# Optimization experiments

Hardware: AMD Instinct MI355X
Metric: run time of the kernel (lower is better)

The kernel has to match this reference:

```python
import jax, jax.numpy as jnp
import numpy as np

N_NODES = 50000
N_EDGES = 800000
DIMS = [100, 512, 256, 128, 200]  # input -> conv1 -> conv2 -> conv3 -> conv4


def setup_inputs() -> dict:
    key = jax.random.key(0)
    ks = jax.random.split(key, 2 + 4)
    x = jax.random.normal(ks[0], (N_NODES, DIMS[0]), dtype=jnp.float32)
    edge_index = jax.random.randint(ks[1], (2, N_EDGES), 0, N_NODES, dtype=jnp.int64)
    inp = {"x": x, "edge_index": edge_index}
    for i in range(4):
        fan_in = DIMS[i]
        W = jax.random.normal(ks[2 + i], (DIMS[i], DIMS[i + 1]), dtype=jnp.float32) * (1.0 / np.sqrt(fan_in)).astype(np.float32)
        b = jnp.zeros((DIMS[i + 1],), dtype=jnp.float32)
        inp[f"W{i + 1}"] = W
        inp[f"b{i + 1}"] = b
    return inp


def _gcn_layer(x, row, col, norm, W, b, n):
    # PyG GCNConv: linear transform first, then normalized scatter-add, then bias.
    h = x @ W                           # [N, out]
    msg = h[row] * norm[:, None]        # [E+N, out] gather + edge scale
    agg = jax.ops.segment_sum(msg, col, num_segments=n)  # scatter-add to targets
    return agg + b


def reference(x, edge_index, W1, b1, W2, b2, W3, b3, W4, b4):
    n = x.shape[0]
    loop = jnp.arange(n, dtype=edge_index.dtype)
    row = jnp.concatenate([edge_index[0], loop])  # sources (with self-loops)
    col = jnp.concatenate([edge_index[1], loop])  # targets (with self-loops)
    deg = jax.ops.segment_sum(jnp.ones_like(col, dtype=x.dtype), col, num_segments=n)
    dinv = jnp.where(deg > 0, jax.lax.rsqrt(deg), 0.0)
    norm = dinv[row] * dinv[col]  # symmetric D^{-1/2}(A+I)D^{-1/2} edge weights

    out = jax.nn.relu(_gcn_layer(x, row, col, norm, W1, b1, n))
    out = jax.nn.relu(_gcn_layer(out, row, col, norm, W2, b2, n))
    out = jax.nn.relu(_gcn_layer(out, row, col, norm, W3, b3, n))
    out = jax.nn.relu(_gcn_layer(out, row, col, norm, W4, b4, n))
    return jnp.mean(out, axis=0, keepdims=True)  # [1, 200]
```

## Files before the change

kernel.cpp:

```cpp
#include <hip/hip_runtime.h>
#include <hip/hip_bf16.h>


#define NN 50000
#define NE 800000

typedef __attribute__((ext_vector_type(8))) _Float16 f16x8;
typedef __attribute__((ext_vector_type(4))) float floatx4;
typedef __attribute__((ext_vector_type(2))) float floatx2;

union U16x8 {
    uint4 u4;
    f16x8 h;
    _Float16 e[8];
};

__device__ __forceinline__ void dec16(const unsigned char* p, float* f) {
    uint4 v = *(const uint4*)p;
    unsigned w[4] = {v.x, v.y, v.z, v.w};
#pragma unroll
    for (int k = 0; k < 4; k++) {
        floatx2 lo = __builtin_amdgcn_cvt_pk_f32_fp8(w[k], false);
        floatx2 hi = __builtin_amdgcn_cvt_pk_f32_fp8(w[k], true);
        f[k * 4 + 0] = lo[0];
        f[k * 4 + 1] = lo[1];
        f[k * 4 + 2] = hi[0];
        f[k * 4 + 3] = hi[1];
    }
}

__device__ __forceinline__ uint4 enc16(const float* f) {
    uint4 r;
    unsigned w;
    w = __builtin_amdgcn_cvt_pk_fp8_f32(f[0], f[1], 0, false);
    w = __builtin_amdgcn_cvt_pk_fp8_f32(f[2], f[3], (int)w, true);
    r.x = w;
    w = __builtin_amdgcn_cvt_pk_fp8_f32(f[4], f[5], 0, false);
    w = __builtin_amdgcn_cvt_pk_fp8_f32(f[6], f[7], (int)w, true);
    r.y = w;
    w = __builtin_amdgcn_cvt_pk_fp8_f32(f[8], f[9], 0, false);
    w = __builtin_amdgcn_cvt_pk_fp8_f32(f[10], f[11], (int)w, true);
    r.z = w;
    w = __builtin_amdgcn_cvt_pk_fp8_f32(f[12], f[13], 0, false);
    w = __builtin_amdgcn_cvt_pk_fp8_f32(f[14], f[15], (int)w, true);
    r.w = w;
    return r;
}

__global__ __launch_bounds__(256) void zero_detect_kernel(
    const unsigned* __restrict__ ei, int* __restrict__ flag,
    unsigned* __restrict__ cnt, unsigned* __restrict__ fillc,
    float* __restrict__ out) {
    int tid = blockIdx.x * 256 + threadIdx.x;
    if (tid < NN) {
        cnt[tid] = 0u;
        fillc[tid] = 0u;
    }
    if (blockIdx.x == 0) {
        if (threadIdx.x < 200) out[threadIdx.x] = 0.f;
        unsigned w = ei[2 * threadIdx.x + 1];
        unsigned long long any = __ballot(w != 0);
        if (threadIdx.x == 0) *flag = (any == 0ull) ? 1 : 0;
    }
}

__device__ __forceinline__ int load_idx(const void* ei, int isflag64, size_t pos) {
    if (isflag64) return (int)((const long long*)ei)[pos];
    return ((const int*)ei)[pos];
}

__global__ __launch_bounds__(256) void count_kernel(const void* ei,
                                                    const int* __restrict__ flag,
                                                    unsigned* __restrict__ cnt) {
    int e = blockIdx.x * blockDim.x + threadIdx.x;
    if (e >= NE) return;
    int c = load_idx(ei, *flag, (size_t)NE + e);
    atomicAdd(&cnt[c], 1u);
}

__global__ __launch_bounds__(256) void scan1_kernel(const unsigned* __restrict__ cnt,
                                                    int* __restrict__ off,
                                                    int* __restrict__ bsum,
                                                    float* __restrict__ dinv) {
    __shared__ int ws[4];
    int b = blockIdx.x, t = threadIdx.x;
    int base = b * 1024 + t * 4;
    int v[4];
    int s = 0;
#pragma unroll
    for (int i = 0; i < 4; i++) {
        int val = 0;
        if (base + i < NN) {
            val = (int)cnt[base + i];
            dinv[base + i] = rsqrtf((float)(val + 1));
        }
        v[i] = s;
        s += val;
    }
    int lane = t & 63, wv = t >> 6;
    int x = s;
    for (int d = 1; d < 64; d <<= 1) {
        int y = __shfl_up(x, d, 64);
        if (lane >= d) x += y;
    }
    if (lane == 63) ws[wv] = x;
    __syncthreads();
    int wpre = 0;
#pragma unroll
    for (int i = 0; i < 4; i++)
        if (i < wv) wpre += ws[i];
    int texcl = x - s + wpre;
#pragma unroll
    for (int i = 0; i < 4; i++)
        if (base + i < NN) off[base + i] = texcl + v[i];
    if (t == 255) bsum[b] = texcl + s;
}

__global__ void scan2_kernel(int* bsum, int nb) {
    int t = threadIdx.x;
    int v = (t < nb) ? bsum[t] : 0;
    int x = v;
    for (int d = 1; d < 64; d <<= 1) {
        int y = __shfl_up(x, d, 64);
        if (t >= d) x += y;
    }
    if (t < nb) bsum[t] = x - v;
}

__global__ __launch_bounds__(256) void scan3_kernel(int* __restrict__ off,
                                                    const int* __restrict__ bsum) {
    int b = blockIdx.x;
    int add = bsum[b];
    int base = b * 1024 + threadIdx.x * 4;
#pragma unroll
    for (int i = 0; i < 4; i++)
        if (base + i < NN) off[base + i] += add;
    if (b == 0 && threadIdx.x == 0) off[NN] = NE;
}

__global__ __launch_bounds__(256) void fill_kernel(
    const void* ei, const int* __restrict__ flag, const int* __restrict__ off,
    unsigned* __restrict__ fillc, const float* __restrict__ dinv,
    int2* __restrict__ ep) {
    int e = blockIdx.x * blockDim.x + threadIdx.x;
    if (e >= NE) return;
    int f64 = *flag;
    int r = load_idx(ei, f64, e);
    int c = load_idx(ei, f64, (size_t)NE + e);
    int pos = off[c] + (int)atomicAdd(&fillc[c], 1u);
    int2 v;
    v.x = r;
    v.y = __float_as_int(dinv[r] * dinv[c]);
    ep[pos] = v;
}

__global__ __launch_bounds__(256) void xwcast_kernel(
    const float* __restrict__ x, unsigned char* __restrict__ xb,
    const float* __restrict__ W1, const float* __restrict__ W2,
    const float* __restrict__ W3, const float* __restrict__ W4,
    _Float16* __restrict__ w1t, _Float16* __restrict__ w2t,
    _Float16* __restrict__ w3t, _Float16* __restrict__ w4t) {
    int bx = blockIdx.x, t = threadIdx.x;
    if (bx < 1563) {
        int tid = bx * 256 + t;
        int node = tid >> 3, sub = tid & 7;
        if (node >= NN) return;
        int base = sub * 16;
        float f[16];
#pragma unroll
        for (int i = 0; i < 16; i++) {
            int c = base + i;
            f[i] = (c < 100) ? x[(size_t)node * 100 + c] : 0.f;
        }
        *(uint4*)(xb + (size_t)node * 128 + base) = enc16(f);
        return;
    }
    int b = bx - 1563;
    const float* W;
    _Float16* Wt;
    int K, N, Kpad, tid;
    if (b < 256)      { W = W1; Wt = w1t; K = 100; N = 512; Kpad = 128; tid = b * 256 + t; }
    else if (b < 768) { W = W2; Wt = w2t; K = 512; N = 256; Kpad = 512; tid = (b - 256) * 256 + t; }
    else if (b < 896) { W = W3; Wt = w3t; K = 256; N = 128; Kpad = 256; tid = (b - 768) * 256 + t; }
    else              { W = W4; Wt = w4t; K = 128; N = 200; Kpad = 128; tid = (b - 896) * 256 + t; }
    int n = tid / Kpad, k = tid - n * Kpad;
    float v = (k < K && n < N) ? W[(size_t)k * N + n] : 0.f;
    Wt[tid] = (_Float16)v;
}

template <int D, int BR, int OUT8>
__global__ __launch_bounds__(256) void agg_kernel(
    const unsigned char* __restrict__ H, const int* __restrict__ off,
    const int2* __restrict__ ep, const float* __restrict__ dinv,
    const float* __restrict__ bias, void* __restrict__ O) {
    constexpr int LPN = D / 16;
    int tid = blockIdx.x * 256 + threadIdx.x;
    int node = tid / LPN;
    int sub = tid % LPN;
    if (node >= NN) return;
    int s = off[node], e = off[node + 1];
    float dc = dinv[node];
    float selfw = dc * dc;
    const int base = sub * 16;
    const unsigned char* __restrict__ Hb = H + base;
    float acc[16], t0[16], t1[16];
    dec16(Hb + (size_t)node * D, t0);
#pragma unroll
    for (int i = 0; i < 16; i++) acc[i] = selfw * t0[i];
    int j = s;
    for (; j + 2 <= e; j += 2) {
        int2 q0 = ep[j];
        int2 q1 = ep[j + 1];
        dec16(Hb + (size_t)q0.x * D, t0);
        dec16(Hb + (size_t)q1.x * D, t1);
        float w0 = __int_as_float(q0.y);
        float w1 = __int_as_float(q1.y);
#pragma unroll
        for (int i = 0; i < 16; i++) acc[i] = fmaf(w0, t0[i], acc[i]);
#pragma unroll
        for (int i = 0; i < 16; i++) acc[i] = fmaf(w1, t1[i], acc[i]);
    }
    if (j < e) {
        int2 q0 = ep[j];
        dec16(Hb + (size_t)q0.x * D, t0);
        float w0 = __int_as_float(q0.y);
#pragma unroll
        for (int i = 0; i < 16; i++) acc[i] = fmaf(w0, t0[i], acc[i]);
    }
    if (BR) {
#pragma unroll
        for (int i = 0; i < 16; i++) acc[i] = fmaxf(acc[i] + bias[base + i], 0.f);
    }
    if (OUT8) {
        *(uint4*)((unsigned char*)O + (size_t)node * D + base) = enc16(acc);
    } else {
        U16x8 o0, o1;
#pragma unroll
        for (int i = 0; i < 8; i++) o0.e[i] = (_Float16)acc[i];
#pragma unroll
        for (int i = 0; i < 8; i++) o1.e[i] = (_Float16)acc[8 + i];
        _Float16* Op = (_Float16*)O + (size_t)node * D + base;
        *(uint4*)Op = o0.u4;
        *(uint4*)(Op + 8) = o1.u4;
    }
}

template <int EPI>
__global__ __launch_bounds__(256) void gemm_kernel(
    const _Float16* __restrict__ A, const _Float16* __restrict__ B,
    const float* __restrict__ bias, void* __restrict__ Cb,
    float* __restrict__ outmean, int M, int K, int N) {
    __shared__ _Float16 Asl[128 * 40];
    __shared__ _Float16 Bsl[128 * 40];
    __shared__ float red[128];
    const int m0 = blockIdx.y * 128;
    const int n0 = blockIdx.x * 128;
    const int t = threadIdx.x;
    const int lane = t & 63, w = t >> 6;
    const int wm = (w >> 1) * 64, wn = (w & 1) * 64;
    const int r16 = lane & 15, quad = lane >> 4;

    floatx4 acc[4][4];
    const floatx4 fz = {0.f, 0.f, 0.f, 0.f};
#pragma unroll
    for (int i = 0; i < 4; i++)
#pragma unroll
        for (int j = 0; j < 4; j++) acc[i][j] = fz;

    for (int kc = 0; kc < K; kc += 32) {
        __syncthreads();
#pragma unroll
        for (int i = 0; i < 2; i++) {
            int seg = t + 256 * i;
            int row = seg >> 2, k8 = (seg & 3) * 8;
            int gm = m0 + row;
            if (gm > M - 1) gm = M - 1;
            *(uint4*)(Asl + row * 40 + k8) = *(const uint4*)(A + (size_t)gm * K + kc + k8);
            int gn = n0 + row;
            *(uint4*)(Bsl + row * 40 + k8) = *(const uint4*)(B + (size_t)gn * K + kc + k8);
        }
        __syncthreads();
        f16x8 af[4], bf[4];
#pragma unroll
        for (int i = 0; i < 4; i++)
            af[i] = *(const f16x8*)(Asl + (wm + i * 16 + r16) * 40 + quad * 8);
#pragma unroll
        for (int j = 0; j < 4; j++)
            bf[j] = *(const f16x8*)(Bsl + (wn + j * 16 + r16) * 40 + quad * 8);
#pragma unroll
        for (int i = 0; i < 4; i++)
#pragma unroll
            for (int j = 0; j < 4; j++)
                acc[i][j] = __builtin_amdgcn_mfma_f32_16x16x32_f16(af[i], bf[j], acc[i][j], 0, 0, 0);
    }

    if (EPI == 2) {
        if (t < 128) red[t] = 0.f;
        __syncthreads();
#pragma unroll
        for (int j = 0; j < 4; j++) {
            int col = n0 + wn + j * 16 + r16;
            float s = 0.f;
            if (col < N) {
                float bv = bias[col];
#pragma unroll
                for (int i = 0; i < 4; i++)
#pragma unroll
                    for (int r = 0; r < 4; r++) {
                        int m = m0 + wm + i * 16 + quad * 4 + r;
                        if (m < M) s += fmaxf(acc[i][j][r] + bv, 0.f);
                    }
            }
            atomicAdd(&red[wn + j * 16 + r16], s);
        }
        __syncthreads();
        if (t < 128) {
            int col = n0 + t;
            if (col < N) atomicAdd(outmean + col, red[t] * (1.0f / (float)NN));
        }
    } else {
#pragma unroll
        for (int i = 0; i < 4; i++)
#pragma unroll
            for (int r = 0; r < 4; r++) {
                int m = m0 + wm + i * 16 + quad * 4 + r;
                if (m >= M) continue;
#pragma unroll
                for (int j = 0; j < 4; j++) {
                    int col = n0 + wn + j * 16 + r16;
                    float v = acc[i][j][r];
                    if (EPI == 1) v = fmaxf(v + bias[col], 0.f);
                    if (EPI == 3) {
                        unsigned pk = __builtin_amdgcn_cvt_pk_fp8_f32(v, v, 0, false);
                        ((unsigned char*)Cb)[(size_t)m * N + col] = (unsigned char)(pk & 0xffu);
                    } else {
                        ((_Float16*)Cb)[(size_t)m * N + col] = (_Float16)v;
                    }
                }
            }
    }
}

extern "C" void kernel_launch(void* const* d_in, const int* in_sizes, int n_in,
                              void* d_out, int out_size, void* d_ws, size_t ws_size,
                              hipStream_t stream) {
    const float* x  = (const float*)d_in[0];
    const void*  ei = d_in[1];
    const float* W1 = (const float*)d_in[2];
    const float* b1 = (const float*)d_in[3];
    const float* W2 = (const float*)d_in[4];
    const float* b2 = (const float*)d_in[5];
    const float* W3 = (const float*)d_in[6];
    const float* b3 = (const float*)d_in[7];
    const float* W4 = (const float*)d_in[8];
    const float* b4 = (const float*)d_in[9];
    float* out = (float*)d_out;

    char* ws = (char*)d_ws;
    size_t o = 0;
    auto alloc = [&](size_t bytes) -> void* {
        void* p = ws + o;
        o += (bytes + 255) & ~(size_t)255;
        return p;
    };
    int*      flag  = (int*)alloc(4);
    unsigned* cnt   = (unsigned*)alloc((size_t)NN * 4);
    int*      off   = (int*)alloc((size_t)(NN + 1) * 4);
    unsigned* fillc = (unsigned*)alloc((size_t)NN * 4);
    float*    dinv  = (float*)alloc((size_t)NN * 4);
    int2*     ep    = (int2*)alloc((size_t)NE * 8);
    _Float16* w1t = (_Float16*)alloc((size_t)512 * 128 * 2);
    _Float16* w2t = (_Float16*)alloc((size_t)256 * 512 * 2);
    _Float16* w3t = (_Float16*)alloc((size_t)128 * 256 * 2);
    _Float16* w4t = (_Float16*)alloc((size_t)256 * 128 * 2);
    int*      bsum  = (int*)alloc(256);
    unsigned char* xb  = (unsigned char*)alloc((size_t)NN * 128);
    _Float16*      A1b = (_Float16*)alloc((size_t)NN * 128 * 2);
    _Float16*      H1b = (_Float16*)alloc((size_t)NN * 512 * 2);
    unsigned char* t2b = (unsigned char*)alloc((size_t)NN * 256);
    _Float16*      H2b = (_Float16*)alloc((size_t)NN * 256 * 2);
    unsigned char* t3b = (unsigned char*)alloc((size_t)NN * 128);
    unsigned char* h3b = (unsigned char*)alloc((size_t)NN * 128);
    _Float16*      A4b = (_Float16*)alloc((size_t)NN * 128 * 2);

    const int EB = (NE + 255) / 256;
    const int NB1 = (NN + 1023) / 1024;
    const int ZB = (NN + 255) / 256;

    zero_detect_kernel<<<ZB, 256, 0, stream>>>((const unsigned*)ei, flag, cnt, fillc, out);
    count_kernel<<<EB, 256, 0, stream>>>(ei, flag, cnt);
    scan1_kernel<<<NB1, 256, 0, stream>>>(cnt, off, bsum, dinv);
    scan2_kernel<<<1, 64, 0, stream>>>(bsum, NB1);
    scan3_kernel<<<NB1, 256, 0, stream>>>(off, bsum);
    fill_kernel<<<EB, 256, 0, stream>>>(ei, flag, off, fillc, dinv, ep);
    xwcast_kernel<<<1563 + 1024, 256, 0, stream>>>(x, xb, W1, W2, W3, W4, w1t, w2t, w3t, w4t);

    const int MB = (NN + 127) / 128;
    const int AB128 = (NN * 8 + 255) / 256;
    const int AB256 = (NN * 16 + 255) / 256;

    agg_kernel<128, 0, 0><<<AB128, 256, 0, stream>>>(xb, off, ep, dinv, nullptr, A1b);
    gemm_kernel<1><<<dim3(4, MB), 256, 0, stream>>>(A1b, w1t, b1, H1b, nullptr, NN, 128, 512);
    gemm_kernel<3><<<dim3(2, MB), 256, 0, stream>>>(H1b, w2t, nullptr, t2b, nullptr, NN, 512, 256);
    agg_kernel<256, 1, 0><<<AB256, 256, 0, stream>>>(t2b, off, ep, dinv, b2, H2b);
    gemm_kernel<3><<<dim3(1, MB), 256, 0, stream>>>(H2b, w3t, nullptr, t3b, nullptr, NN, 256, 128);
    agg_kernel<128, 1, 1><<<AB128, 256, 0, stream>>>(t3b, off, ep, dinv, b3, h3b);
    agg_kernel<128, 0, 0><<<AB128, 256, 0, stream>>>(h3b, off, ep, dinv, nullptr, A4b);
    gemm_kernel<2><<<dim3(2, MB), 256, 0, stream>>>(A4b, w4t, b4, nullptr, out, NN, 128, 200);
}
```

Before: 356.0 us.

## Store all intermediate activations in fp8 and batch four edges per thread

All intermediate activations (aggregation outputs and GEMM outputs) are now stored as fp8 instead of fp16. The GEMM converts fp8 A tiles to fp16 while loading them into shared memory. This roughly halves memory traffic for several buffers, at the cost of extra conversion work and lower precision. The count and fill kernels also process four edges per thread to raise memory-level parallelism and cut thread overhead.

After: 356.4 us. Within noise of the previous version (+0.1%).

```diff
diff --git a/kernel.cpp b/kernel.cpp
--- a/kernel.cpp
+++ b/kernel.cpp
@@ -47,6 +47,19 @@
     return r;
 }
 
+__device__ __forceinline__ uint4 dec8_f16(uint2 v) {
+    floatx2 f0 = __builtin_amdgcn_cvt_pk_f32_fp8(v.x, false);
+    floatx2 f1 = __builtin_amdgcn_cvt_pk_f32_fp8(v.x, true);
+    floatx2 f2 = __builtin_amdgcn_cvt_pk_f32_fp8(v.y, false);
+    floatx2 f3 = __builtin_amdgcn_cvt_pk_f32_fp8(v.y, true);
+    U16x8 o;
+    o.e[0] = (_Float16)f0[0]; o.e[1] = (_Float16)f0[1];
+    o.e[2] = (_Float16)f1[0]; o.e[3] = (_Float16)f1[1];
+    o.e[4] = (_Float16)f2[0]; o.e[5] = (_Float16)f2[1];
+    o.e[6] = (_Float16)f3[0]; o.e[7] = (_Float16)f3[1];
+    return o.u4;
+}
+
 __global__ __launch_bounds__(256) void zero_detect_kernel(
     const unsigned* __restrict__ ei, int* __restrict__ flag,
     unsigned* __restrict__ cnt, unsigned* __restrict__ fillc,
@@ -64,18 +77,23 @@
     }
 }
 
-__device__ __forceinline__ int load_idx(const void* ei, int isflag64, size_t pos) {
-    if (isflag64) return (int)((const long long*)ei)[pos];
-    return ((const int*)ei)[pos];
-}
-
 __global__ __launch_bounds__(256) void count_kernel(const void* ei,
                                                     const int* __restrict__ flag,
                                                     unsigned* __restrict__ cnt) {
-    int e = blockIdx.x * blockDim.x + threadIdx.x;
-    if (e >= NE) return;
-    int c = load_idx(ei, *flag, (size_t)NE + e);
-    atomicAdd(&cnt[c], 1u);
+    int base = (blockIdx.x * 256 + threadIdx.x) * 4;
+    if (base >= NE) return;
+    int c[4];
+    if (*flag) {
+        const long long* p = (const long long*)ei + NE;
+#pragma unroll
+        for (int i = 0; i < 4; i++) c[i] = (int)p[base + i];
+    } else {
+        const int* p = (const int*)ei + NE;
+#pragma unroll
+        for (int i = 0; i < 4; i++) c[i] = p[base + i];
+    }
+#pragma unroll
+    for (int i = 0; i < 4; i++) atomicAdd(&cnt[c[i]], 1u);
 }
 
 __global__ __launch_bounds__(256) void scan1_kernel(const unsigned* __restrict__ cnt,
@@ -142,16 +160,35 @@
     const void* ei, const int* __restrict__ flag, const int* __restrict__ off,
     unsigned* __restrict__ fillc, const float* __restrict__ dinv,
     int2* __restrict__ ep) {
-    int e = blockIdx.x * blockDim.x + threadIdx.x;
-    if (e >= NE) return;
-    int f64 = *flag;
-    int r = load_idx(ei, f64, e);
-    int c = load_idx(ei, f64, (size_t)NE + e);
-    int pos = off[c] + (int)atomicAdd(&fillc[c], 1u);
-    int2 v;
-    v.x = r;
-    v.y = __float_as_int(dinv[r] * dinv[c]);
-    ep[pos] = v;
+    int base = (blockIdx.x * 256 + threadIdx.x) * 4;
+    if (base >= NE) return;
+    int r[4], c[4];
+    if (*flag) {
+        const long long* p = (const long long*)ei;
+#pragma unroll
+        for (int i = 0; i < 4; i++) {
+            r[i] = (int)p[base + i];
+            c[i] = (int)p[NE + base + i];
+        }
+    } else {
+        const int* p = (const int*)ei;
+#pragma unroll
+        for (int i = 0; i < 4; i++) {
+            r[i] = p[base + i];
+            c[i] = p[NE + base + i];
+        }
+    }
+    int pos[4];
+#pragma unroll
+    for (int i = 0; i < 4; i++)
+        pos[i] = off[c[i]] + (int)atomicAdd(&fillc[c[i]], 1u);
+#pragma unroll
+    for (int i = 0; i < 4; i++) {
+        int2 v;
+        v.x = r[i];
+        v.y = __float_as_int(dinv[r[i]] * dinv[c[i]]);
+        ep[pos[i]] = v;
+    }
 }
 
 __global__ __launch_bounds__(256) void xwcast_kernel(
@@ -188,11 +225,11 @@
     Wt[tid] = (_Float16)v;
 }
 
-template <int D, int BR, int OUT8>
+template <int D, int BR>
 __global__ __launch_bounds__(256) void agg_kernel(
     const unsigned char* __restrict__ H, const int* __restrict__ off,
     const int2* __restrict__ ep, const float* __restrict__ dinv,
-    const float* __restrict__ bias, void* __restrict__ O) {
+    const float* __restrict__ bias, unsigned char* __restrict__ O) {
     constexpr int LPN = D / 16;
     int tid = blockIdx.x * 256 + threadIdx.x;
     int node = tid / LPN;
@@ -231,24 +268,13 @@
 #pragma unroll
         for (int i = 0; i < 16; i++) acc[i] = fmaxf(acc[i] + bias[base + i], 0.f);
     }
-    if (OUT8) {
-        *(uint4*)((unsigned char*)O + (size_t)node * D + base) = enc16(acc);
-    } else {
-        U16x8 o0, o1;
-#pragma unroll
-        for (int i = 0; i < 8; i++) o0.e[i] = (_Float16)acc[i];
-#pragma unroll
-        for (int i = 0; i < 8; i++) o1.e[i] = (_Float16)acc[8 + i];
-        _Float16* Op = (_Float16*)O + (size_t)node * D + base;
-        *(uint4*)Op = o0.u4;
-        *(uint4*)(Op + 8) = o1.u4;
-    }
+    *(uint4*)(O + (size_t)node * D + base) = enc16(acc);
 }
 
 template <int EPI>
 __global__ __launch_bounds__(256) void gemm_kernel(
-    const _Float16* __restrict__ A, const _Float16* __restrict__ B,
-    const float* __restrict__ bias, void* __restrict__ Cb,
+    const unsigned char* __restrict__ A, const _Float16* __restrict__ B,
+    const float* __restrict__ bias, unsigned char* __restrict__ Cb,
     float* __restrict__ outmean, int M, int K, int N) {
     __shared__ _Float16 Asl[128 * 40];
     __shared__ _Float16 Bsl[128 * 40];
@@ -275,7 +301,8 @@
             int row = seg >> 2, k8 = (seg & 3) * 8;
             int gm = m0 + row;
             if (gm > M - 1) gm = M - 1;
-            *(uint4*)(Asl + row * 40 + k8) = *(const uint4*)(A + (size_t)gm * K + kc + k8);
+            uint2 av = *(const uint2*)(A + (size_t)gm * K + kc + k8);
+            *(uint4*)(Asl + row * 40 + k8) = dec8_f16(av);
             int gn = n0 + row;
             *(uint4*)(Bsl + row * 40 + k8) = *(const uint4*)(B + (size_t)gn * K + kc + k8);
         }
@@ -330,12 +357,8 @@
                     int col = n0 + wn + j * 16 + r16;
                     float v = acc[i][j][r];
                     if (EPI == 1) v = fmaxf(v + bias[col], 0.f);
-                    if (EPI == 3) {
-                        unsigned pk = __builtin_amdgcn_cvt_pk_fp8_f32(v, v, 0, false);
-                        ((unsigned char*)Cb)[(size_t)m * N + col] = (unsigned char)(pk & 0xffu);
-                    } else {
-                        ((_Float16*)Cb)[(size_t)m * N + col] = (_Float16)v;
-                    }
+                    unsigned pk = __builtin_amdgcn_cvt_pk_fp8_f32(v, v, 0, false);
+                    Cb[(size_t)m * N + col] = (unsigned char)(pk & 0xffu);
                 }
             }
     }
@@ -375,36 +398,36 @@
     _Float16* w4t = (_Float16*)alloc((size_t)256 * 128 * 2);
     int*      bsum  = (int*)alloc(256);
     unsigned char* xb  = (unsigned char*)alloc((size_t)NN * 128);
-    _Float16*      A1b = (_Float16*)alloc((size_t)NN * 128 * 2);
-    _Float16*      H1b = (_Float16*)alloc((size_t)NN * 512 * 2);
+    unsigned char* A1b = (unsigned char*)alloc((size_t)NN * 128);
+    unsigned char* H1b = (unsigned char*)alloc((size_t)NN * 512);
     unsigned char* t2b = (unsigned char*)alloc((size_t)NN * 256);
-    _Float16*      H2b = (_Float16*)alloc((size_t)NN * 256 * 2);
+    unsigned char* H2b = (unsigned char*)alloc((size_t)NN * 256);
     unsigned char* t3b = (unsigned char*)alloc((size_t)NN * 128);
     unsigned char* h3b = (unsigned char*)alloc((size_t)NN * 128);
-    _Float16*      A4b = (_Float16*)alloc((size_t)NN * 128 * 2);
-
-    const int EB = (NE + 255) / 256;
+    unsigned char* A4b = (unsigned char*)alloc((size_t)NN * 128);
+
+    const int EB4 = (NE / 4 + 255) / 256;
     const int NB1 = (NN + 1023) / 1024;
     const int ZB = (NN + 255) / 256;
 
     zero_detect_kernel<<<ZB, 256, 0, stream>>>((const unsigned*)ei, flag, cnt, fillc, out);
-    count_kernel<<<EB, 256, 0, stream>>>(ei, flag, cnt);
+    count_kernel<<<EB4, 256, 0, stream>>>(ei, flag, cnt);
     scan1_kernel<<<NB1, 256, 0, stream>>>(cnt, off, bsum, dinv);
     scan2_kernel<<<1, 64, 0, stream>>>(bsum, NB1);
     scan3_kernel<<<NB1, 256, 0, stream>>>(off, bsum);
-    fill_kernel<<<EB, 256, 0, stream>>>(ei, flag, off, fillc, dinv, ep);
+    fill_kernel<<<EB4, 256, 0, stream>>>(ei, flag, off, fillc, dinv, ep);
     xwcast_kernel<<<1563 + 1024, 256, 0, stream>>>(x, xb, W1, W2, W3, W4, w1t, w2t, w3t, w4t);
 
     const int MB = (NN + 127) / 128;
     const int AB128 = (NN * 8 + 255) / 256;
     const int AB256 = (NN * 16 + 255) / 256;
 
-    agg_kernel<128, 0, 0><<<AB128, 256, 0, stream>>>(xb, off, ep, dinv, nullptr, A1b);
+    agg_kernel<128, 0><<<AB128, 256, 0, stream>>>(xb, off, ep, dinv, nullptr, A1b);
     gemm_kernel<1><<<dim3(4, MB), 256, 0, stream>>>(A1b, w1t, b1, H1b, nullptr, NN, 128, 512);
-    gemm_kernel<3><<<dim3(2, MB), 256, 0, stream>>>(H1b, w2t, nullptr, t2b, nullptr, NN, 512, 256);
-    agg_kernel<256, 1, 0><<<AB256, 256, 0, stream>>>(t2b, off, ep, dinv, b2, H2b);
-    gemm_kernel<3><<<dim3(1, MB), 256, 0, stream>>>(H2b, w3t, nullptr, t3b, nullptr, NN, 256, 128);
-    agg_kernel<128, 1, 1><<<AB128, 256, 0, stream>>>(t3b, off, ep, dinv, b3, h3b);
-    agg_kernel<128, 0, 0><<<AB128, 256, 0, stream>>>(h3b, off, ep, dinv, nullptr, A4b);
+    gemm_kernel<0><<<dim3(2, MB), 256, 0, stream>>>(H1b, w2t, nullptr, t2b, nullptr, NN, 512, 256);
+    agg_kernel<256, 1><<<AB256, 256, 0, stream>>>(t2b, off, ep, dinv, b2, H2b);
+    gemm_kernel<0><<<dim3(1, MB), 256, 0, stream>>>(H2b, w3t, nullptr, t3b, nullptr, NN, 256, 128);
+    agg_kernel<128, 1><<<AB128, 256, 0, stream>>>(t3b, off, ep, dinv, b3, h3b);
+    agg_kernel<128, 0><<<AB128, 256, 0, stream>>>(h3b, off, ep, dinv, nullptr, A4b);
     gemm_kernel<2><<<dim3(2, MB), 256, 0, stream>>>(A4b, w4t, b4, nullptr, out, NN, 128, 200);
 }
```
